# Kernel tuning notes

Measured on AMD Instinct MI355X. Metric: run time of the kernel, lower is better.

## Reference

```python
import jax, jax.numpy as jnp
import numpy as np

B, S, IN_DIM, HID = 128, 512, 512, 1024


def setup_inputs() -> dict:
    key = jax.random.key(0)
    k0, k1, k2, k3, k4 = jax.random.split(key, 5)
    s_ih = 1.0 / np.sqrt(HID)
    return {
        "embedding_sequence": jax.random.normal(k0, (B, S, IN_DIM), dtype=jnp.float32),
        "w_ih": jax.random.uniform(k1, (3 * HID, IN_DIM), jnp.float32, -s_ih, s_ih),
        "w_hh": jax.random.uniform(k2, (3 * HID, HID), jnp.float32, -s_ih, s_ih),
        "b_ih": jax.random.uniform(k3, (3 * HID,), jnp.float32, -s_ih, s_ih),
        "b_hh": jax.random.uniform(k4, (3 * HID,), jnp.float32, -s_ih, s_ih),
    }


def _gru_scan(embedding_sequence, w_ih, w_hh, b_ih, b_hh):
    # Precompute input-side gate projections for all steps: [B,S,3H]
    gi_all = jnp.einsum('bsi,gi->bsg', embedding_sequence, w_ih) + b_ih

    def step(h, gi):
        gh = h @ w_hh.T + b_hh                      # [B,3H]
        i_r, i_z, i_n = jnp.split(gi, 3, axis=-1)
        h_r, h_z, h_n = jnp.split(gh, 3, axis=-1)
        r = jax.nn.sigmoid(i_r + h_r)
        z = jax.nn.sigmoid(i_z + h_z)
        n = jnp.tanh(i_n + r * h_n)
        h_new = (1.0 - z) * n + z * h
        return h_new, h_new

    h0 = jnp.zeros((embedding_sequence.shape[0], HID), dtype=embedding_sequence.dtype)
    h_last, hiddens = jax.lax.scan(step, h0, jnp.swapaxes(gi_all, 0, 1))
    return jnp.swapaxes(hiddens, 0, 1), h_last      # ([B,S,H], [B,H])


def reference(embedding_sequence, w_ih, w_hh, b_ih, b_hh):
    return _gru_scan(embedding_sequence, w_ih, w_hh, b_ih, b_hh)
```

## Files before the change

kernel.cpp:

```cpp
#include <hip/hip_runtime.h>
#include <hip/hip_bf16.h>

#define BB   128
#define SS   512
#define IND  512
#define HID  1024
#define NBLK 256
#define GRPBLK 64
#define NSTRIPE 8

#define WHH_LD (HID + 8)
#define WIH_LD (IND + 8)

typedef __attribute__((ext_vector_type(8))) short s8v;
typedef __attribute__((ext_vector_type(4))) float f4v;
typedef unsigned long long u64;
typedef unsigned int u32;

__device__ __forceinline__ short f2bf(float f) {
    union { float f; u32 u; } v; v.f = f;
    u32 u = v.u + 0x7FFFu + ((v.u >> 16) & 1u);
    return (short)(u >> 16);
}


__global__ void __launch_bounds__(128, 1)
gru_persistent(const float* __restrict__ X,
               const float* __restrict__ Wih,
               const float* __restrict__ Whh,
               const float* __restrict__ bih,
               const float* __restrict__ bhh,
               float* __restrict__ out,
               short* __restrict__ bufA,
               short* __restrict__ bufB,
               u64*   __restrict__ ctr)
{
    __shared__ __align__(16) short whh_lds[48 * WHH_LD];
    __shared__ __align__(16) short wih_lds[48 * WIH_LD];

    const int tid  = threadIdx.x;
    const int wave = tid >> 6;
    const int lane = tid & 63;
    const int blk  = blockIdx.x;
    const int mi   = blk >> 6;
    const int jg   = blk & 63;

    for (int idx = tid; idx < 48 * (HID / 4); idx += 128) {
        int s = idx / (HID / 4), k4 = idx % (HID / 4);
        int grow = (s >> 4) * HID + jg * 16 + (s & 15);
        float4 v = *(const float4*)(Whh + (size_t)grow * HID + k4 * 4);
        short* d = &whh_lds[s * WHH_LD + k4 * 4];
        d[0] = f2bf(v.x); d[1] = f2bf(v.y); d[2] = f2bf(v.z); d[3] = f2bf(v.w);
    }
    for (int idx = tid; idx < 48 * (IND / 4); idx += 128) {
        int s = idx / (IND / 4), k4 = idx % (IND / 4);
        int grow = (s >> 4) * HID + jg * 16 + (s & 15);
        float4 v = *(const float4*)(Wih + (size_t)grow * IND + k4 * 4);
        short* d = &wih_lds[s * WIH_LD + k4 * 4];
        d[0] = f2bf(v.x); d[1] = f2bf(v.y); d[2] = f2bf(v.z); d[3] = f2bf(v.w);
    }

    const int n  = lane & 15;
    const int kg = lane >> 4;
    const int j  = jg * 16 + n;
    const float bir = bih[j], biz = bih[HID + j], bin_ = bih[2 * HID + j];
    const float bhr = bhh[j], bhz = bhh[HID + j], bhn  = bhh[2 * HID + j];

    const int rowbase = mi * 32 + wave * 16;
    const int wg      = mi * 2 + wave;

    const int wkk = j >> 5, wkg = (j >> 3) & 3;
    const u32 rest   = (u32)wkk * 1024u + (u32)wkg * 256u
                     + (u32)kg * 64u + ((u32)(n & 7) << 1);
    const u32 wbyteA = (u32)wg * 32768u + rest;
    const u32 wbyteB = (u32)mi * 131072u + (u32)(wg & 1) * 32768u + rest;

    const u64* hbA = (const u64*)bufA + (size_t)wg * 4096 + lane * 2;
    const u64* hbB = (const u64*)bufB + (size_t)mi * 16384
                   + (size_t)(wg & 1) * 4096 + lane * 2;

    float hkeep[4] = {0.f, 0.f, 0.f, 0.f};

    __syncthreads();

    for (int t = 0; t < SS; ++t) {
        f4v acc_r  = {0.f,0.f,0.f,0.f};
        f4v acc_z  = {0.f,0.f,0.f,0.f};
        f4v acc_in = {0.f,0.f,0.f,0.f};
        f4v acc_hn = {0.f,0.f,0.f,0.f};

        {
            const float* xrow = X + ((size_t)(rowbase + n) * SS + t) * IND;
            #pragma unroll 4
            for (int kk = 0; kk < IND / 32; ++kk) {
                const int k0 = kk * 32 + kg * 8;
                const float4* px = (const float4*)(xrow + k0);
                float4 x0 = px[0], x1 = px[1];
                s8v a;
                a[0]=f2bf(x0.x); a[1]=f2bf(x0.y); a[2]=f2bf(x0.z); a[3]=f2bf(x0.w);
                a[4]=f2bf(x1.x); a[5]=f2bf(x1.y); a[6]=f2bf(x1.z); a[7]=f2bf(x1.w);
                s8v br = *(const s8v*)&wih_lds[(0 * 16 + n) * WIH_LD + k0];
                s8v bz = *(const s8v*)&wih_lds[(1 * 16 + n) * WIH_LD + k0];
                s8v bn = *(const s8v*)&wih_lds[(2 * 16 + n) * WIH_LD + k0];
                acc_r  = __builtin_amdgcn_mfma_f32_16x16x32_bf16(a, br, acc_r,  0,0,0);
                acc_z  = __builtin_amdgcn_mfma_f32_16x16x32_bf16(a, bz, acc_z,  0,0,0);
                acc_in = __builtin_amdgcn_mfma_f32_16x16x32_bf16(a, bn, acc_in, 0,0,0);
            }
        }

        if (t > 0) {
            const u64* hb = (t & 1) ? hbA : hbB;
            s8v areg[32];
            #pragma unroll
            for (int q = 0; q < 8; ++q) {
                u64 lo = __hip_atomic_load(hb + q * 128,
                                           __ATOMIC_RELAXED, __HIP_MEMORY_SCOPE_AGENT);
                u64 hi = __hip_atomic_load(hb + q * 128 + 1,
                                           __ATOMIC_RELAXED, __HIP_MEMORY_SCOPE_AGENT);
                union { u64 qq[2]; s8v v; } u; u.qq[0] = lo; u.qq[1] = hi;
                areg[q] = u.v;
            }
            __builtin_amdgcn_sched_barrier(0);
            #pragma unroll
            for (int c = 0; c < 4; ++c) {
                if (c < 3) {
                    #pragma unroll
                    for (int q = 0; q < 8; ++q) {
                        const int kk = (c + 1) * 8 + q;
                        u64 lo = __hip_atomic_load(hb + kk * 128,
                                                   __ATOMIC_RELAXED, __HIP_MEMORY_SCOPE_AGENT);
                        u64 hi = __hip_atomic_load(hb + kk * 128 + 1,
                                                   __ATOMIC_RELAXED, __HIP_MEMORY_SCOPE_AGENT);
                        union { u64 qq[2]; s8v v; } u; u.qq[0] = lo; u.qq[1] = hi;
                        areg[kk] = u.v;
                    }
                }
                __builtin_amdgcn_sched_barrier(0);
                #pragma unroll
                for (int q = 0; q < 8; ++q) {
                    const int kk = c * 8 + q;
                    const int k0 = kk * 32 + kg * 8;
                    s8v br = *(const s8v*)&whh_lds[(0 * 16 + n) * WHH_LD + k0];
                    s8v bz = *(const s8v*)&whh_lds[(1 * 16 + n) * WHH_LD + k0];
                    s8v bn = *(const s8v*)&whh_lds[(2 * 16 + n) * WHH_LD + k0];
                    acc_r  = __builtin_amdgcn_mfma_f32_16x16x32_bf16(areg[kk], br, acc_r,  0,0,0);
                    acc_z  = __builtin_amdgcn_mfma_f32_16x16x32_bf16(areg[kk], bz, acc_z,  0,0,0);
                    acc_hn = __builtin_amdgcn_mfma_f32_16x16x32_bf16(areg[kk], bn, acc_hn, 0,0,0);
                }
                __builtin_amdgcn_sched_barrier(0);
            }
        }

        u64 pack2[4];
        float hnew4[4];
        #pragma unroll
        for (int r = 0; r < 4; ++r) {
            float gr = acc_r[r] + bir + bhr;
            float gz = acc_z[r] + biz + bhz;
            float rr = 1.f / (1.f + __expf(-gr));
            float zz = 1.f / (1.f + __expf(-gz));
            float hn = acc_hn[r] + bhn;
            float na = acc_in[r] + bin_ + rr * hn;
            float e2 = __expf(2.f * na);
            float nn = (e2 - 1.f) / (e2 + 1.f);
            float hnew = (1.f - zz) * nn + zz * hkeep[r];
            hkeep[r] = hnew;
            hnew4[r] = hnew;
            u32 hb16 = (u32)(unsigned short)f2bf(hnew);
            u32 p = hb16 | ((u32)__shfl_xor((int)hb16, 1) << 16);
            u32 q = (u32)__shfl_xor((int)p, 2);
            pack2[r] = (u64)p | ((u64)q << 32);
        }
        #pragma unroll
        for (int r = 0; r < 4; ++r) {
            const int b = rowbase + kg * 4 + r;
            out[(size_t)b * (SS * HID) + (size_t)t * HID + j] = hnew4[r];
            if (t == SS - 1)
                out[(size_t)BB * SS * HID + (size_t)b * HID + j] = hnew4[r];
        }

        if (t < SS - 1) {
            if (!(n & 3)) {
                char* base = (t & 1) ? ((char*)bufB + wbyteB) : ((char*)bufA + wbyteA);
                #pragma unroll
                for (int r = 0; r < 4; ++r)
                    __hip_atomic_store((u64*)(base + r * 16), pack2[r],
                                       __ATOMIC_RELAXED, __HIP_MEMORY_SCOPE_AGENT);
            }
            __syncthreads();
            if (tid == 0) {
                __hip_atomic_fetch_add(&ctr[(mi * NSTRIPE + (blk & 7)) * 8], 1ull,
                                       __ATOMIC_RELAXED, __HIP_MEMORY_SCOPE_AGENT);
                const u64 target = (u64)GRPBLK * (u64)(t + 1);
                for (;;) {
                    u64 s = 0;
                    #pragma unroll
                    for (int i = 0; i < NSTRIPE; ++i)
                        s += __hip_atomic_load(&ctr[(mi * NSTRIPE + i) * 8],
                                               __ATOMIC_RELAXED,
                                               __HIP_MEMORY_SCOPE_AGENT);
                    if (s >= target) break;
                    __builtin_amdgcn_s_sleep(1);
                }
            }
            __syncthreads();
        }
    }
}

extern "C" void kernel_launch(void* const* d_in, const int* in_sizes, int n_in,
                              void* d_out, int out_size, void* d_ws, size_t ws_size,
                              hipStream_t stream) {
    const float* X   = (const float*)d_in[0];
    const float* Wih = (const float*)d_in[1];
    const float* Whh = (const float*)d_in[2];
    const float* bih = (const float*)d_in[3];
    const float* bhh = (const float*)d_in[4];
    float* out = (float*)d_out;

    u64*   ctr  = (u64*)d_ws;
    short* bufA = (short*)((char*)d_ws + 4096);
    short* bufB = (short*)(out + (size_t)BB * SS * HID);

    hipMemsetAsync(d_ws, 0, 4096, stream);

    void* args[] = { (void*)&X, (void*)&Wih, (void*)&Whh, (void*)&bih,
                     (void*)&bhh, (void*)&out, (void*)&bufA, (void*)&bufB,
                     (void*)&ctr };
    hipLaunchCooperativeKernel((const void*)gru_persistent,
                               dim3(NBLK), dim3(128), args, 0, stream);
}
```

Measured before the change: 3.795 ms.

## Pre-swizzle weights in LDS into MFMA fragment order and defer output stores

Weights are now laid out in LDS so that each lane's 16-byte MFMA B-fragment sits contiguously, indexed by (kk, lane). This replaces the padded row-major layout and simplifies address math and LDS access patterns. The per-step global store of the hidden state is also moved to the start of the next step, so it no longer sits on the critical path before the publish-and-barrier. The last step's output and h_last are written in a separate branch.

After: 3.870 ms. Within noise of the previous version (+2.0%).

```diff
diff --git a/kernel.cpp b/kernel.cpp
--- a/kernel.cpp
+++ b/kernel.cpp
@@ -8,9 +8,6 @@
 #define NBLK 256
 #define GRPBLK 64
 #define NSTRIPE 8
-
-#define WHH_LD (HID + 8)
-#define WIH_LD (IND + 8)
 
 typedef __attribute__((ext_vector_type(8))) short s8v;
 typedef __attribute__((ext_vector_type(4))) float f4v;
@@ -35,8 +32,8 @@
                short* __restrict__ bufB,
                u64*   __restrict__ ctr)
 {
-    __shared__ __align__(16) short whh_lds[48 * WHH_LD];
-    __shared__ __align__(16) short wih_lds[48 * WIH_LD];
+    __shared__ __align__(16) short whh2[3 * 32 * 64 * 8];
+    __shared__ __align__(16) short wih2[3 * 16 * 64 * 8];
 
     const int tid  = threadIdx.x;
     const int wave = tid >> 6;
@@ -46,19 +43,32 @@
     const int jg   = blk & 63;
 
     for (int idx = tid; idx < 48 * (HID / 4); idx += 128) {
-        int s = idx / (HID / 4), k4 = idx % (HID / 4);
-        int grow = (s >> 4) * HID + jg * 16 + (s & 15);
+        int s = idx >> 8, k4 = idx & 255;
+        int g = s >> 4, n_ = s & 15;
+        int grow = g * HID + jg * 16 + n_;
         float4 v = *(const float4*)(Whh + (size_t)grow * HID + k4 * 4);
-        short* d = &whh_lds[s * WHH_LD + k4 * 4];
+        int k  = k4 * 4;
+        int kk = k >> 5, kg_ = (k >> 3) & 3, e0 = k & 7;
+        short* d = &whh2[(((g * 32 + kk) * 64) + (kg_ * 16 + n_)) * 8 + e0];
         d[0] = f2bf(v.x); d[1] = f2bf(v.y); d[2] = f2bf(v.z); d[3] = f2bf(v.w);
     }
     for (int idx = tid; idx < 48 * (IND / 4); idx += 128) {
-        int s = idx / (IND / 4), k4 = idx % (IND / 4);
-        int grow = (s >> 4) * HID + jg * 16 + (s & 15);
+        int s = idx >> 7, k4 = idx & 127;
+        int g = s >> 4, n_ = s & 15;
+        int grow = g * HID + jg * 16 + n_;
         float4 v = *(const float4*)(Wih + (size_t)grow * IND + k4 * 4);
-        short* d = &wih_lds[s * WIH_LD + k4 * 4];
+        int k  = k4 * 4;
+        int kk = k >> 5, kg_ = (k >> 3) & 3, e0 = k & 7;
+        short* d = &wih2[(((g * 16 + kk) * 64) + (kg_ * 16 + n_)) * 8 + e0];
         d[0] = f2bf(v.x); d[1] = f2bf(v.y); d[2] = f2bf(v.z); d[3] = f2bf(v.w);
     }
+
+    const short* wihr = wih2;
+    const short* wihz = wih2 + 16 * 64 * 8;
+    const short* wihn = wih2 + 2 * 16 * 64 * 8;
+    const short* whhr = whh2;
+    const short* whhz = whh2 + 32 * 64 * 8;
+    const short* whhn = whh2 + 2 * 32 * 64 * 8;
 
     const int n  = lane & 15;
     const int kg = lane >> 4;
@@ -84,6 +94,14 @@
     __syncthreads();
 
     for (int t = 0; t < SS; ++t) {
+        if (t > 0) {
+            #pragma unroll
+            for (int r = 0; r < 4; ++r) {
+                const int b = rowbase + kg * 4 + r;
+                out[(size_t)b * (SS * HID) + (size_t)(t - 1) * HID + j] = hkeep[r];
+            }
+        }
+
         f4v acc_r  = {0.f,0.f,0.f,0.f};
         f4v acc_z  = {0.f,0.f,0.f,0.f};
         f4v acc_in = {0.f,0.f,0.f,0.f};
@@ -99,9 +117,9 @@
                 s8v a;
                 a[0]=f2bf(x0.x); a[1]=f2bf(x0.y); a[2]=f2bf(x0.z); a[3]=f2bf(x0.w);
                 a[4]=f2bf(x1.x); a[5]=f2bf(x1.y); a[6]=f2bf(x1.z); a[7]=f2bf(x1.w);
-                s8v br = *(const s8v*)&wih_lds[(0 * 16 + n) * WIH_LD + k0];
-                s8v bz = *(const s8v*)&wih_lds[(1 * 16 + n) * WIH_LD + k0];
-                s8v bn = *(const s8v*)&wih_lds[(2 * 16 + n) * WIH_LD + k0];
+                s8v br = *(const s8v*)&wihr[((kk << 6) | lane) << 3];
+                s8v bz = *(const s8v*)&wihz[((kk << 6) | lane) << 3];
+                s8v bn = *(const s8v*)&wihn[((kk << 6) | lane) << 3];
                 acc_r  = __builtin_amdgcn_mfma_f32_16x16x32_bf16(a, br, acc_r,  0,0,0);
                 acc_z  = __builtin_amdgcn_mfma_f32_16x16x32_bf16(a, bz, acc_z,  0,0,0);
                 acc_in = __builtin_amdgcn_mfma_f32_16x16x32_bf16(a, bn, acc_in, 0,0,0);
@@ -139,10 +157,9 @@
                 #pragma unroll
                 for (int q = 0; q < 8; ++q) {
                     const int kk = c * 8 + q;
-                    const int k0 = kk * 32 + kg * 8;
-                    s8v br = *(const s8v*)&whh_lds[(0 * 16 + n) * WHH_LD + k0];
-                    s8v bz = *(const s8v*)&whh_lds[(1 * 16 + n) * WHH_LD + k0];
-                    s8v bn = *(const s8v*)&whh_lds[(2 * 16 + n) * WHH_LD + k0];
+                    s8v br = *(const s8v*)&whhr[((kk << 6) | lane) << 3];
+                    s8v bz = *(const s8v*)&whhz[((kk << 6) | lane) << 3];
+                    s8v bn = *(const s8v*)&whhn[((kk << 6) | lane) << 3];
                     acc_r  = __builtin_amdgcn_mfma_f32_16x16x32_bf16(areg[kk], br, acc_r,  0,0,0);
                     acc_z  = __builtin_amdgcn_mfma_f32_16x16x32_bf16(areg[kk], bz, acc_z,  0,0,0);
                     acc_hn = __builtin_amdgcn_mfma_f32_16x16x32_bf16(areg[kk], bn, acc_hn, 0,0,0);
@@ -152,7 +169,6 @@
         }
 
         u64 pack2[4];
-        float hnew4[4];
         #pragma unroll
         for (int r = 0; r < 4; ++r) {
             float gr = acc_r[r] + bir + bhr;
@@ -165,18 +181,10 @@
             float nn = (e2 - 1.f) / (e2 + 1.f);
             float hnew = (1.f - zz) * nn + zz * hkeep[r];
             hkeep[r] = hnew;
-            hnew4[r] = hnew;
             u32 hb16 = (u32)(unsigned short)f2bf(hnew);
             u32 p = hb16 | ((u32)__shfl_xor((int)hb16, 1) << 16);
             u32 q = (u32)__shfl_xor((int)p, 2);
             pack2[r] = (u64)p | ((u64)q << 32);
-        }
-        #pragma unroll
-        for (int r = 0; r < 4; ++r) {
-            const int b = rowbase + kg * 4 + r;
-            out[(size_t)b * (SS * HID) + (size_t)t * HID + j] = hnew4[r];
-            if (t == SS - 1)
-                out[(size_t)BB * SS * HID + (size_t)b * HID + j] = hnew4[r];
         }
 
         if (t < SS - 1) {
@@ -204,6 +212,13 @@
                 }
             }
             __syncthreads();
+        } else {
+            #pragma unroll
+            for (int r = 0; r < 4; ++r) {
+                const int b = rowbase + kg * 4 + r;
+                out[(size_t)b * (SS * HID) + (size_t)t * HID + j] = hkeep[r];
+                out[(size_t)BB * SS * HID + (size_t)b * HID + j] = hkeep[r];
+            }
         }
     }
 }
```
